# Performance work log

Hardware: AMD Instinct MI355X
Metric: run time of the kernel (lower is better)

Reference implementation:

```python
import jax, jax.numpy as jnp
import numpy as np

N_NODES = 100000
N_EDGES = 500000
NODE_IN = 16
HID = 128
EDGE_IN = 1
NUM_STACKED = 4  # layers 1..4 share shapes; layer 0 maps NODE_IN -> HID


def setup_inputs() -> dict:
    key = jax.random.key(0)
    ks = jax.random.split(key, 16)

    def p(k, shape, fan_in):
        return (jax.random.normal(k, shape, dtype=jnp.float32) / np.float32(np.sqrt(fan_in)))

    inp = {}
    inp["x"] = jax.random.normal(ks[0], (N_NODES, NODE_IN), dtype=jnp.float32)
    inp["edge_index"] = jax.random.randint(ks[1], (2, N_EDGES), 0, N_NODES)
    inp["edge_attr"] = jax.random.normal(ks[2], (N_EDGES, EDGE_IN), dtype=jnp.float32)
    # GINE layer 0 (NODE_IN -> HID): edge lin maps EDGE_IN -> NODE_IN (PyG GINEConv.lin)
    inp["We0"] = p(ks[3], (EDGE_IN, NODE_IN), EDGE_IN)
    inp["be0"] = jnp.zeros((NODE_IN,), jnp.float32)
    inp["W10"] = p(ks[4], (NODE_IN, HID), NODE_IN)
    inp["b10"] = jnp.zeros((HID,), jnp.float32)
    inp["W20"] = p(ks[5], (HID, HID), HID)
    inp["b20"] = jnp.zeros((HID,), jnp.float32)
    # GINE layers 1..4 (HID -> HID), stacked on leading axis
    inp["We_s"] = p(ks[6], (NUM_STACKED, EDGE_IN, HID), EDGE_IN)
    inp["be_s"] = jnp.zeros((NUM_STACKED, HID), jnp.float32)
    inp["W1_s"] = p(ks[7], (NUM_STACKED, HID, HID), HID)
    inp["b1_s"] = jnp.zeros((NUM_STACKED, HID), jnp.float32)
    inp["W2_s"] = p(ks[8], (NUM_STACKED, HID, HID), HID)
    inp["b2_s"] = jnp.zeros((NUM_STACKED, HID), jnp.float32)
    # edge predictor: Linear(2*HID, HID) -> ELU -> Linear(HID, 1)
    inp["Wp1"] = p(ks[9], (2 * HID, HID), 2 * HID)
    inp["bp1"] = jnp.zeros((HID,), jnp.float32)
    inp["Wp2"] = p(ks[10], (HID, 1), HID)
    inp["bp2"] = jnp.zeros((1,), jnp.float32)
    return inp


def _gine(x, src, dst, eattr, We, be, W1, b1, W2, b2):
    # PyG GINEConv: aggr_i = sum_{(j->i)} ReLU(x_j + lin(edge_attr)); out = nn((1+eps)*x + aggr), eps=0
    m = jax.nn.relu(x[src] + eattr @ We + be)                 # [E, d] gathered messages
    aggr = jax.ops.segment_sum(m, dst, num_segments=x.shape[0])  # scatter-add to targets
    h = x + aggr
    return jax.nn.elu(h @ W1 + b1) @ W2 + b2                  # nn = Linear-ELU-Linear


def reference(x, edge_index, edge_attr, We0, be0, W10, b10, W20, b20,
              We_s, be_s, W1_s, b1_s, W2_s, b2_s, Wp1, bp1, Wp2, bp2):
    src, dst = edge_index[0], edge_index[1]
    # dropout is identity at inference (eval mode)
    h = jax.nn.elu(_gine(x, src, dst, edge_attr, We0, be0, W10, b10, W20, b20))
    for l in range(NUM_STACKED):
        h = jax.nn.elu(_gine(h, src, dst, edge_attr,
                             We_s[l], be_s[l], W1_s[l], b1_s[l], W2_s[l], b2_s[l]))
    ef = jnp.concatenate([h[src], h[dst]], axis=1)            # [E, 2*HID]
    out = jax.nn.elu(ef @ Wp1 + bp1) @ Wp2 + bp2              # [E, 1]
    return out[:, 0]
```

## Files before the change

kernel.cpp:

```cpp
#include <hip/hip_runtime.h>

#define N_NODES 100000
#define N_EDGES 500000
#define NODE_IN 16
#define HID 128
#define LPAD 140
#define SCAN_CHUNK 1024
#define NB_SCAN ((N_NODES + SCAN_CHUNK - 1) / SCAN_CHUNK)

typedef __attribute__((ext_vector_type(8))) short short8;
typedef __attribute__((ext_vector_type(4))) float f32x4;

__device__ __forceinline__ float elu_f(float v) {
    return v > 0.f ? v : __expf(v) - 1.f;
}

__device__ __forceinline__ unsigned short f2b(float f) {
    unsigned int u = __float_as_uint(f);
    unsigned int r = (u + 0x7fffu + ((u >> 16) & 1u)) >> 16;
    return (unsigned short)r;
}
__device__ __forceinline__ float b2f(unsigned short h) {
    return __uint_as_float((unsigned int)h << 16);
}
__device__ __forceinline__ unsigned short f2h(float f) {
    _Float16 h = (_Float16)f;
    unsigned short u;
    __builtin_memcpy(&u, &h, 2);
    return u;
}
__device__ __forceinline__ float h2f(unsigned short u) {
    _Float16 h;
    __builtin_memcpy(&h, &u, 2);
    return (float)h;
}

__global__ void deg_count_kernel(const int* __restrict__ ei, int* __restrict__ deg) {
    int e = blockIdx.x * 256 + threadIdx.x;
    if (e < N_EDGES) atomicAdd(&deg[ei[N_EDGES + e]], 1);
}

__global__ __launch_bounds__(1024) void scanA_kernel(const int* __restrict__ deg, int* __restrict__ bsum) {
    __shared__ int s[SCAN_CHUNK];
    int i = blockIdx.x * SCAN_CHUNK + threadIdx.x;
    s[threadIdx.x] = (i < N_NODES) ? deg[i] : 0;
    __syncthreads();
    for (int off = SCAN_CHUNK / 2; off > 0; off >>= 1) {
        if (threadIdx.x < off) s[threadIdx.x] += s[threadIdx.x + off];
        __syncthreads();
    }
    if (threadIdx.x == 0) bsum[blockIdx.x] = s[0];
}

__global__ void scanB_kernel(const int* __restrict__ bsum, int* __restrict__ boff,
                             int* __restrict__ rowPtr) {
    if (threadIdx.x == 0 && blockIdx.x == 0) {
        int r = 0;
        for (int i = 0; i < NB_SCAN; i++) { boff[i] = r; r += bsum[i]; }
        rowPtr[N_NODES] = N_EDGES;
    }
}

__global__ __launch_bounds__(1024) void scanC_kernel(const int* __restrict__ deg,
                                                     const int* __restrict__ boff,
                                                     int* __restrict__ rowPtr,
                                                     int* __restrict__ cursor) {
    __shared__ int bufA[SCAN_CHUNK], bufB[SCAN_CHUNK];
    int i = blockIdx.x * SCAN_CHUNK + threadIdx.x;
    int t = threadIdx.x;
    bufA[t] = (i < N_NODES) ? deg[i] : 0;
    __syncthreads();
    int* src = bufA; int* dst = bufB;
    for (int off = 1; off < SCAN_CHUNK; off <<= 1) {
        dst[t] = (t >= off) ? (src[t - off] + src[t]) : src[t];
        __syncthreads();
        int* tmp = src; src = dst; dst = tmp;
    }
    if (i < N_NODES) {
        int excl = (t == 0) ? 0 : src[t - 1];
        int v = excl + boff[blockIdx.x];
        rowPtr[i] = v;
        cursor[i] = v;
    }
}

__global__ void fill_kernel(const int* __restrict__ ei, const float* __restrict__ ea,
                            int* __restrict__ cursor, int2* __restrict__ edgeP) {
    int e = blockIdx.x * 256 + threadIdx.x;
    if (e < N_EDGES) {
        int d = ei[N_EDGES + e];
        int p = atomicAdd(&cursor[d], 1);
        edgeP[p] = make_int2(ei[e], __float_as_int(ea[e]));
    }
}

__global__ __launch_bounds__(256) void pack_w_kernel(const float* __restrict__ W, int K_off,
                                                     unsigned short* __restrict__ hi,
                                                     unsigned short* __restrict__ lo)
{
    int gid = blockIdx.x * 256 + threadIdx.x;
    if (gid >= 4 * 8 * 64) return;
    int lane = gid & 63, tl = (gid >> 6) & 7, ch = gid >> 9;
    int kb = ch * 32 + (lane >> 4) * 8;
    int n  = tl * 16 + (lane & 15);
    for (int j = 0; j < 8; j++) {
        float w = W[(size_t)(K_off + kb + j) * 128 + n];
        unsigned short h = f2b(w);
        hi[(size_t)gid * 8 + j] = h;
        lo[(size_t)gid * 8 + j] = f2b(w - b2f(h));
    }
}

__global__ __launch_bounds__(256) void scatter0_kernel(
    const float* __restrict__ x, const int* __restrict__ ei,
    const float* __restrict__ ea, const float* __restrict__ We0,
    const float* __restrict__ be0, float* __restrict__ aggr)
{
    int idx = blockIdx.x * 256 + threadIdx.x;
    int e = idx >> 4, c = idx & 15;
    int s = ei[e], d = ei[N_EDGES + e];
    float m = x[s * NODE_IN + c] + ea[e] * We0[c] + be0[c];
    m = fmaxf(m, 0.f);
    atomicAdd(&aggr[d * NODE_IN + c], m);
}

__device__ __forceinline__ void fma4x4(float (&acc)[4][4],
    const float4& r0, const float4& r1, const float4& r2, const float4& r3,
    const float4& w0, const float4& w1, const float4& w2, const float4& w3)
{
    float r[4][4] = {{r0.x, r0.y, r0.z, r0.w}, {r1.x, r1.y, r1.z, r1.w},
                     {r2.x, r2.y, r2.z, r2.w}, {r3.x, r3.y, r3.z, r3.w}};
    float w[4][4] = {{w0.x, w0.y, w0.z, w0.w}, {w1.x, w1.y, w1.z, w1.w},
                     {w2.x, w2.y, w2.z, w2.w}, {w3.x, w3.y, w3.z, w3.w}};
#pragma unroll
    for (int i = 0; i < 4; i++)
#pragma unroll
        for (int k = 0; k < 4; k++)
#pragma unroll
            for (int c = 0; c < 4; c++)
                acc[i][c] = fmaf(r[i][k], w[k][c], acc[i][c]);
}

__global__ __launch_bounds__(256) void mlp0_kernel(
    const float* __restrict__ x, const float* __restrict__ aggr,
    const float* __restrict__ W1, const float* __restrict__ b1,
    const float* __restrict__ W2, const float* __restrict__ b2,
    unsigned short* __restrict__ h)
{
    __shared__ float in0[32][20];
    __shared__ float mid[32][HID];
    const int t = threadIdx.x;
    const int q = t & 31, g = t >> 5;
    const int c0 = q * 4;
    const int base = blockIdx.x * 32;

    for (int i = t; i < 32 * NODE_IN; i += 256) {
        int r = i >> 4, cc = i & 15;
        int n = base + r;
        in0[r][cc] = x[n * NODE_IN + cc] + aggr[n * NODE_IN + cc];
    }
    __syncthreads();

    float4 bb = *(const float4*)&b1[c0];
    float acc[4][4];
#pragma unroll
    for (int i = 0; i < 4; i++) { acc[i][0] = bb.x; acc[i][1] = bb.y; acc[i][2] = bb.z; acc[i][3] = bb.w; }
    for (int k = 0; k < NODE_IN; k += 4) {
        float4 r0 = *(const float4*)&in0[g * 4 + 0][k];
        float4 r1 = *(const float4*)&in0[g * 4 + 1][k];
        float4 r2 = *(const float4*)&in0[g * 4 + 2][k];
        float4 r3 = *(const float4*)&in0[g * 4 + 3][k];
        float4 w0 = *(const float4*)&W1[(k + 0) * HID + c0];
        float4 w1 = *(const float4*)&W1[(k + 1) * HID + c0];
        float4 w2 = *(const float4*)&W1[(k + 2) * HID + c0];
        float4 w3 = *(const float4*)&W1[(k + 3) * HID + c0];
        fma4x4(acc, r0, r1, r2, r3, w0, w1, w2, w3);
    }
#pragma unroll
    for (int i = 0; i < 4; i++)
        *(float4*)&mid[g * 4 + i][c0] = make_float4(elu_f(acc[i][0]), elu_f(acc[i][1]),
                                                    elu_f(acc[i][2]), elu_f(acc[i][3]));
    __syncthreads();

    float4 bb2 = *(const float4*)&b2[c0];
    float acc2[4][4];
#pragma unroll
    for (int i = 0; i < 4; i++) { acc2[i][0] = bb2.x; acc2[i][1] = bb2.y; acc2[i][2] = bb2.z; acc2[i][3] = bb2.w; }
    for (int k = 0; k < HID; k += 4) {
        float4 r0 = *(const float4*)&mid[g * 4 + 0][k];
        float4 r1 = *(const float4*)&mid[g * 4 + 1][k];
        float4 r2 = *(const float4*)&mid[g * 4 + 2][k];
        float4 r3 = *(const float4*)&mid[g * 4 + 3][k];
        float4 w0 = *(const float4*)&W2[(k + 0) * HID + c0];
        float4 w1 = *(const float4*)&W2[(k + 1) * HID + c0];
        float4 w2 = *(const float4*)&W2[(k + 2) * HID + c0];
        float4 w3 = *(const float4*)&W2[(k + 3) * HID + c0];
        fma4x4(acc2, r0, r1, r2, r3, w0, w1, w2, w3);
    }
#pragma unroll
    for (int i = 0; i < 4; i++) {
        ushort4 o;
        o.x = f2h(elu_f(acc2[i][0])); o.y = f2h(elu_f(acc2[i][1]));
        o.z = f2h(elu_f(acc2[i][2])); o.w = f2h(elu_f(acc2[i][3]));
        *(ushort4*)&h[(size_t)(base + g * 4 + i) * HID + c0] = o;
    }
}

__device__ __forceinline__ void afrag_split(const float (&buf)[16][LPAD], int lane,
                                            short8 (&ah)[4], short8 (&al)[4])
{
    const int m = lane & 15, s8 = (lane >> 4) * 8;
#pragma unroll
    for (int ch = 0; ch < 4; ch++) {
        float4 a0 = *(const float4*)&buf[m][ch * 32 + s8];
        float4 a1 = *(const float4*)&buf[m][ch * 32 + s8 + 4];
        float av[8] = {a0.x, a0.y, a0.z, a0.w, a1.x, a1.y, a1.z, a1.w};
#pragma unroll
        for (int j = 0; j < 8; j++) {
            unsigned short h = f2b(av[j]);
            ah[ch][j] = (short)h;
            al[ch][j] = (short)f2b(av[j] - b2f(h));
        }
    }
}

template <bool PRED>
__global__ __launch_bounds__(64) void gine_mfma_kernel(
    const unsigned short* __restrict__ hin, const int* __restrict__ rowPtr,
    const int2* __restrict__ edgeP,
    const float* __restrict__ We, const float* __restrict__ be,
    const unsigned short* __restrict__ W1h, const unsigned short* __restrict__ W1l,
    const float* __restrict__ b1,
    const unsigned short* __restrict__ W2h, const unsigned short* __restrict__ W2l,
    const float* __restrict__ b2,
    unsigned short* __restrict__ hout,
    const unsigned short* __restrict__ P1h, const unsigned short* __restrict__ P1l,
    const unsigned short* __restrict__ P2h, const unsigned short* __restrict__ P2l,
    unsigned short* __restrict__ Pbuf)
{
    __shared__ float buf[16][LPAD];
    const int lane = threadIdx.x;
    const int qg = lane & 15, rg = lane >> 4;
    const int c0 = qg * 8;
    const int base = blockIdx.x * 16;

    float wev[8], bev[8];
#pragma unroll
    for (int j = 0; j < 8; j++) { wev[j] = We[c0 + j]; bev[j] = be[c0 + j]; }

    int s0[4], e0[4];
    float acc[4][8];
#pragma unroll
    for (int i = 0; i < 4; i++) {
        int n = base + rg * 4 + i;
        s0[i] = rowPtr[n];
        e0[i] = rowPtr[n + 1];
        short8 h0 = *(const short8*)&hin[(size_t)n * HID + c0];
#pragma unroll
        for (int j = 0; j < 8; j++) acc[i][j] = h2f((unsigned short)h0[j]);
    }
    int maxd = 0;
#pragma unroll
    for (int i = 0; i < 4; i++) maxd = max(maxd, e0[i] - s0[i]);

    int idx[8]; float av[8]; bool act[8];
#pragma unroll
    for (int u = 0; u < 2; u++)
#pragma unroll
        for (int i = 0; i < 4; i++) {
            int slot = u * 4 + i;
            int j = s0[i] + u;
            act[slot] = j < e0[i];
            int jc = act[slot] ? j : (N_EDGES - 1);
            int2 ep = edgeP[jc];
            idx[slot] = ep.x;
            av[slot]  = __int_as_float(ep.y);
        }

    for (int sb = 0; sb < maxd; sb += 2) {
        short8 hraw[8];
#pragma unroll
        for (int s = 0; s < 8; s++)
            hraw[s] = *(const short8*)&hin[(size_t)idx[s] * HID + c0];

        int nidx[8]; float nav[8]; bool nact[8];
#pragma unroll
        for (int u = 0; u < 2; u++)
#pragma unroll
            for (int i = 0; i < 4; i++) {
                int slot = u * 4 + i;
                int j = s0[i] + sb + 2 + u;
                nact[slot] = j < e0[i];
                int jc = nact[slot] ? j : (N_EDGES - 1);
                int2 ep = edgeP[jc];
                nidx[slot] = ep.x;
                nav[slot]  = __int_as_float(ep.y);
            }

#pragma unroll
        for (int u = 0; u < 2; u++)
#pragma unroll
            for (int i = 0; i < 4; i++) {
                int slot = u * 4 + i;
                if (act[slot]) {
#pragma unroll
                    for (int j = 0; j < 8; j++) {
                        float hv = h2f((unsigned short)hraw[slot][j]);
                        acc[i][j] += fmaxf(fmaf(av[slot], wev[j], bev[j]) + hv, 0.f);
                    }
                }
            }
#pragma unroll
        for (int s = 0; s < 8; s++) {
            idx[s] = nidx[s]; av[s] = nav[s]; act[s] = nact[s];
        }
    }
#pragma unroll
    for (int i = 0; i < 4; i++) {
        *(float4*)&buf[rg * 4 + i][c0]     = make_float4(acc[i][0], acc[i][1], acc[i][2], acc[i][3]);
        *(float4*)&buf[rg * 4 + i][c0 + 4] = make_float4(acc[i][4], acc[i][5], acc[i][6], acc[i][7]);
    }
    __syncthreads();

    const int col16 = lane & 15, r0 = (lane >> 4) * 4;

    {
        short8 ah[4], al[4];
        afrag_split(buf, lane, ah, al);
        float res[8][4];
#pragma unroll
        for (int tl = 0; tl < 8; tl++) {
            int col = tl * 16 + col16;
            float bv = b1[col];
            f32x4 c = {bv, bv, bv, bv};
#pragma unroll
            for (int ch = 0; ch < 4; ch++) {
                int off = ((ch * 8 + tl) * 64 + lane) * 8;
                short8 bh = *(const short8*)&W1h[off];
                short8 bl = *(const short8*)&W1l[off];
                c = __builtin_amdgcn_mfma_f32_16x16x32_bf16(ah[ch], bh, c, 0, 0, 0);
                c = __builtin_amdgcn_mfma_f32_16x16x32_bf16(al[ch], bh, c, 0, 0, 0);
                c = __builtin_amdgcn_mfma_f32_16x16x32_bf16(ah[ch], bl, c, 0, 0, 0);
            }
#pragma unroll
            for (int r = 0; r < 4; r++) res[tl][r] = elu_f(c[r]);
        }
        __syncthreads();
#pragma unroll
        for (int tl = 0; tl < 8; tl++)
#pragma unroll
            for (int r = 0; r < 4; r++)
                buf[r0 + r][tl * 16 + col16] = res[tl][r];
    }
    __syncthreads();

    {
        short8 ah[4], al[4];
        afrag_split(buf, lane, ah, al);
        float res[8][4];
#pragma unroll
        for (int tl = 0; tl < 8; tl++) {
            int col = tl * 16 + col16;
            float bv = b2[col];
            f32x4 c = {bv, bv, bv, bv};
#pragma unroll
            for (int ch = 0; ch < 4; ch++) {
                int off = ((ch * 8 + tl) * 64 + lane) * 8;
                short8 bh = *(const short8*)&W2h[off];
                short8 bl = *(const short8*)&W2l[off];
                c = __builtin_amdgcn_mfma_f32_16x16x32_bf16(ah[ch], bh, c, 0, 0, 0);
                c = __builtin_amdgcn_mfma_f32_16x16x32_bf16(al[ch], bh, c, 0, 0, 0);
                c = __builtin_amdgcn_mfma_f32_16x16x32_bf16(ah[ch], bl, c, 0, 0, 0);
            }
#pragma unroll
            for (int r = 0; r < 4; r++) res[tl][r] = elu_f(c[r]);
        }
        __syncthreads();
#pragma unroll
        for (int tl = 0; tl < 8; tl++)
#pragma unroll
            for (int r = 0; r < 4; r++)
                buf[r0 + r][tl * 16 + col16] = res[tl][r];
    }
    __syncthreads();

    if constexpr (!PRED) {
#pragma unroll
        for (int i = 0; i < 4; i++) {
            int n = base + rg * 4 + i;
            short8 o;
#pragma unroll
            for (int j = 0; j < 8; j++) o[j] = (short)f2h(buf[rg * 4 + i][c0 + j]);
            *(short8*)&hout[(size_t)n * HID + c0] = o;
        }
    } else {
        short8 ah[4], al[4];
        afrag_split(buf, lane, ah, al);
#pragma unroll
        for (int tl = 0; tl < 8; tl++) {
            int col = tl * 16 + col16;
            f32x4 c1 = {0.f, 0.f, 0.f, 0.f};
            f32x4 c2 = {0.f, 0.f, 0.f, 0.f};
#pragma unroll
            for (int ch = 0; ch < 4; ch++) {
                int off = ((ch * 8 + tl) * 64 + lane) * 8;
                short8 bh1 = *(const short8*)&P1h[off];
                short8 bl1 = *(const short8*)&P1l[off];
                c1 = __builtin_amdgcn_mfma_f32_16x16x32_bf16(ah[ch], bh1, c1, 0, 0, 0);
                c1 = __builtin_amdgcn_mfma_f32_16x16x32_bf16(al[ch], bh1, c1, 0, 0, 0);
                c1 = __builtin_amdgcn_mfma_f32_16x16x32_bf16(ah[ch], bl1, c1, 0, 0, 0);
                short8 bh2 = *(const short8*)&P2h[off];
                short8 bl2 = *(const short8*)&P2l[off];
                c2 = __builtin_amdgcn_mfma_f32_16x16x32_bf16(ah[ch], bh2, c2, 0, 0, 0);
                c2 = __builtin_amdgcn_mfma_f32_16x16x32_bf16(al[ch], bh2, c2, 0, 0, 0);
                c2 = __builtin_amdgcn_mfma_f32_16x16x32_bf16(ah[ch], bl2, c2, 0, 0, 0);
            }
#pragma unroll
            for (int r = 0; r < 4; r++) {
                size_t n = base + r0 + r;
                Pbuf[n * 256 + col]       = f2b(c1[r]);
                Pbuf[n * 256 + 128 + col] = f2b(c2[r]);
            }
        }
    }
}

__global__ __launch_bounds__(256) void pred_edge_kernel(
    const unsigned short* __restrict__ Pbuf, const int* __restrict__ ei,
    const float* __restrict__ bp1, const float* __restrict__ Wp2,
    const float* __restrict__ bp2, float* __restrict__ out)
{
    const int t = threadIdx.x;
    const int lane = t & 31;
    const int eloc = t >> 5;
    const int e = blockIdx.x * 8 + eloc;
    const int c0 = lane * 4;

    int s = ei[e], d = ei[N_EDGES + e];
    ushort4 ua = *(const ushort4*)&Pbuf[(size_t)s * 256 + c0];
    ushort4 ub = *(const ushort4*)&Pbuf[(size_t)d * 256 + 128 + c0];
    float4 bb = *(const float4*)&bp1[c0];
    float4 w = *(const float4*)&Wp2[c0];
    float r = elu_f(b2f(ua.x) + b2f(ub.x) + bb.x) * w.x
            + elu_f(b2f(ua.y) + b2f(ub.y) + bb.y) * w.y
            + elu_f(b2f(ua.z) + b2f(ub.z) + bb.z) * w.z
            + elu_f(b2f(ua.w) + b2f(ub.w) + bb.w) * w.w;
#pragma unroll
    for (int off = 16; off > 0; off >>= 1) r += __shfl_down(r, off, 32);
    if (lane == 0) out[e] = r + bp2[0];
}

extern "C" void kernel_launch(void* const* d_in, const int* in_sizes, int n_in,
                              void* d_out, int out_size, void* d_ws, size_t ws_size,
                              hipStream_t stream) {
    const float* x    = (const float*)d_in[0];
    const int*   ei   = (const int*)d_in[1];
    const float* ea   = (const float*)d_in[2];
    const float* We0  = (const float*)d_in[3];
    const float* be0  = (const float*)d_in[4];
    const float* W10  = (const float*)d_in[5];
    const float* b10  = (const float*)d_in[6];
    const float* W20  = (const float*)d_in[7];
    const float* b20  = (const float*)d_in[8];
    const float* We_s = (const float*)d_in[9];
    const float* be_s = (const float*)d_in[10];
    const float* W1_s = (const float*)d_in[11];
    const float* b1_s = (const float*)d_in[12];
    const float* W2_s = (const float*)d_in[13];
    const float* b2_s = (const float*)d_in[14];
    const float* Wp1  = (const float*)d_in[15];
    const float* bp1  = (const float*)d_in[16];
    const float* Wp2  = (const float*)d_in[17];
    const float* bp2  = (const float*)d_in[18];
    float* out = (float*)d_out;

    unsigned short* h16A = (unsigned short*)d_ws;
    unsigned short* h16B = h16A + (size_t)N_NODES * HID;
    unsigned short* Pbuf = h16B + (size_t)N_NODES * HID;
    float* R = (float*)(Pbuf + (size_t)N_NODES * 256);

    float* aggr0 = R;
    int* deg     = (int*)(aggr0 + (size_t)N_NODES * NODE_IN);
    int* rowPtr  = deg + N_NODES;
    int* cursor  = rowPtr + N_NODES + 1;
    int2* edgeP  = (int2*)(cursor + N_NODES);
    int* bsum    = (int*)(edgeP + N_EDGES);
    int* boff    = bsum + NB_SCAN;

    unsigned short* wpk = (unsigned short*)(R + (size_t)6 * 1024 * 1024);
    const size_t WSLOT = 16384;

    hipMemsetAsync(deg, 0, N_NODES * sizeof(int), stream);
    deg_count_kernel<<<(N_EDGES + 255) / 256, 256, 0, stream>>>(ei, deg);
    scanA_kernel<<<NB_SCAN, SCAN_CHUNK, 0, stream>>>(deg, bsum);
    scanB_kernel<<<1, 64, 0, stream>>>(bsum, boff, rowPtr);
    scanC_kernel<<<NB_SCAN, SCAN_CHUNK, 0, stream>>>(deg, boff, rowPtr, cursor);
    fill_kernel<<<(N_EDGES + 255) / 256, 256, 0, stream>>>(ei, ea, cursor, edgeP);

    for (int l = 0; l < 4; l++) {
        pack_w_kernel<<<8, 256, 0, stream>>>(W1_s + (size_t)l * 16384, 0,
                                             wpk + (0 + l) * WSLOT, wpk + (4 + l) * WSLOT);
        pack_w_kernel<<<8, 256, 0, stream>>>(W2_s + (size_t)l * 16384, 0,
                                             wpk + (8 + l) * WSLOT, wpk + (12 + l) * WSLOT);
    }
    pack_w_kernel<<<8, 256, 0, stream>>>(Wp1, 0,   wpk + 16 * WSLOT, wpk + 17 * WSLOT);
    pack_w_kernel<<<8, 256, 0, stream>>>(Wp1, 128, wpk + 18 * WSLOT, wpk + 19 * WSLOT);

    hipMemsetAsync(aggr0, 0, (size_t)N_NODES * NODE_IN * sizeof(float), stream);
    scatter0_kernel<<<(N_EDGES * NODE_IN) / 256, 256, 0, stream>>>(x, ei, ea, We0, be0, aggr0);
    mlp0_kernel<<<N_NODES / 32, 256, 0, stream>>>(x, aggr0, W10, b10, W20, b20, h16A);

    unsigned short* hin = h16A; unsigned short* hout_ = h16B;
    for (int l = 0; l < 3; l++) {
        gine_mfma_kernel<false><<<N_NODES / 16, 64, 0, stream>>>(
            hin, rowPtr, edgeP,
            We_s + l * HID, be_s + l * HID,
            wpk + (0 + l) * WSLOT, wpk + (4 + l) * WSLOT, b1_s + l * HID,
            wpk + (8 + l) * WSLOT, wpk + (12 + l) * WSLOT, b2_s + l * HID,
            hout_, nullptr, nullptr, nullptr, nullptr, nullptr);
        unsigned short* tmp = hin; hin = hout_; hout_ = tmp;
    }

    {
        const int l = 3;
        gine_mfma_kernel<true><<<N_NODES / 16, 64, 0, stream>>>(
            hin, rowPtr, edgeP,
            We_s + l * HID, be_s + l * HID,
            wpk + (0 + l) * WSLOT, wpk + (4 + l) * WSLOT, b1_s + l * HID,
            wpk + (8 + l) * WSLOT, wpk + (12 + l) * WSLOT, b2_s + l * HID,
            nullptr, wpk + 16 * WSLOT, wpk + 17 * WSLOT,
            wpk + 18 * WSLOT, wpk + 19 * WSLOT, Pbuf);
    }

    pred_edge_kernel<<<N_EDGES / 8, 256, 0, stream>>>(Pbuf, ei, bp1, Wp2, bp2, out);
}
```

Before: 616.8 us.

## Sort nodes by in-degree so each GINE block gathers balanced edge counts

Builds a degree histogram, scans it, and produces a permutation that groups nodes by in-degree. The GINE kernels then process nodes in permuted order, so the four nodes sharing a wavefront row group have similar degrees and the maxd loop wastes fewer iterations. This adds three small preprocessing kernels plus a memset, and it makes hin/hout and Pbuf row accesses indirect and scattered rather than contiguous, which costs memory locality.

```diff
diff --git a/kernel.cpp b/kernel.cpp
--- a/kernel.cpp
+++ b/kernel.cpp
@@ -7,6 +7,7 @@
 #define LPAD 140
 #define SCAN_CHUNK 1024
 #define NB_SCAN ((N_NODES + SCAN_CHUNK - 1) / SCAN_CHUNK)
+#define DBINS 1024
 
 typedef __attribute__((ext_vector_type(8))) short short8;
 typedef __attribute__((ext_vector_type(4))) float f32x4;
@@ -91,6 +92,36 @@
         int d = ei[N_EDGES + e];
         int p = atomicAdd(&cursor[d], 1);
         edgeP[p] = make_int2(ei[e], __float_as_int(ea[e]));
+    }
+}
+
+__global__ void hist_kernel(const int* __restrict__ deg, int* __restrict__ hist) {
+    int i = blockIdx.x * 256 + threadIdx.x;
+    if (i < N_NODES) atomicAdd(&hist[min(deg[i], DBINS - 1)], 1);
+}
+
+__global__ __launch_bounds__(1024) void binscan_kernel(const int* __restrict__ hist,
+                                                       int* __restrict__ bcur) {
+    __shared__ int bufA[DBINS], bufB[DBINS];
+    int t = threadIdx.x;
+    bufA[t] = hist[t];
+    __syncthreads();
+    int* src = bufA; int* dst = bufB;
+    for (int off = 1; off < DBINS; off <<= 1) {
+        dst[t] = (t >= off) ? (src[t - off] + src[t]) : src[t];
+        __syncthreads();
+        int* tmp = src; src = dst; dst = tmp;
+    }
+    bcur[t] = (t == 0) ? 0 : src[t - 1];
+}
+
+__global__ void permute_kernel(const int* __restrict__ deg, int* __restrict__ bcur,
+                               int* __restrict__ perm) {
+    int i = blockIdx.x * 256 + threadIdx.x;
+    if (i < N_NODES) {
+        int b = min(deg[i], DBINS - 1);
+        int p = atomicAdd(&bcur[b], 1);
+        perm[p] = i;
     }
 }
 
@@ -227,7 +258,7 @@
 template <bool PRED>
 __global__ __launch_bounds__(64) void gine_mfma_kernel(
     const unsigned short* __restrict__ hin, const int* __restrict__ rowPtr,
-    const int2* __restrict__ edgeP,
+    const int2* __restrict__ edgeP, const int* __restrict__ perm,
     const float* __restrict__ We, const float* __restrict__ be,
     const unsigned short* __restrict__ W1h, const unsigned short* __restrict__ W1l,
     const float* __restrict__ b1,
@@ -248,14 +279,14 @@
 #pragma unroll
     for (int j = 0; j < 8; j++) { wev[j] = We[c0 + j]; bev[j] = be[c0 + j]; }
 
-    int s0[4], e0[4];
+    int nn[4], s0[4], e0[4];
     float acc[4][8];
 #pragma unroll
     for (int i = 0; i < 4; i++) {
-        int n = base + rg * 4 + i;
-        s0[i] = rowPtr[n];
-        e0[i] = rowPtr[n + 1];
-        short8 h0 = *(const short8*)&hin[(size_t)n * HID + c0];
+        nn[i] = perm[base + rg * 4 + i];
+        s0[i] = rowPtr[nn[i]];
+        e0[i] = rowPtr[nn[i] + 1];
+        short8 h0 = *(const short8*)&hin[(size_t)nn[i] * HID + c0];
 #pragma unroll
         for (int j = 0; j < 8; j++) acc[i][j] = h2f((unsigned short)h0[j]);
     }
@@ -387,15 +418,17 @@
     if constexpr (!PRED) {
 #pragma unroll
         for (int i = 0; i < 4; i++) {
-            int n = base + rg * 4 + i;
             short8 o;
 #pragma unroll
             for (int j = 0; j < 8; j++) o[j] = (short)f2h(buf[rg * 4 + i][c0 + j]);
-            *(short8*)&hout[(size_t)n * HID + c0] = o;
+            *(short8*)&hout[(size_t)nn[i] * HID + c0] = o;
         }
     } else {
         short8 ah[4], al[4];
         afrag_split(buf, lane, ah, al);
+        int pn[4];
+#pragma unroll
+        for (int r = 0; r < 4; r++) pn[r] = perm[base + r0 + r];
 #pragma unroll
         for (int tl = 0; tl < 8; tl++) {
             int col = tl * 16 + col16;
@@ -417,7 +450,7 @@
             }
 #pragma unroll
             for (int r = 0; r < 4; r++) {
-                size_t n = base + r0 + r;
+                size_t n = (size_t)pn[r];
                 Pbuf[n * 256 + col]       = f2b(c1[r]);
                 Pbuf[n * 256 + 128 + col] = f2b(c2[r]);
             }
@@ -486,6 +519,9 @@
     int2* edgeP  = (int2*)(cursor + N_NODES);
     int* bsum    = (int*)(edgeP + N_EDGES);
     int* boff    = bsum + NB_SCAN;
+    int* hist    = boff + NB_SCAN;
+    int* bcur    = hist + DBINS;
+    int* perm    = bcur + DBINS;
 
     unsigned short* wpk = (unsigned short*)(R + (size_t)6 * 1024 * 1024);
     const size_t WSLOT = 16384;
@@ -497,6 +533,11 @@
     scanC_kernel<<<NB_SCAN, SCAN_CHUNK, 0, stream>>>(deg, boff, rowPtr, cursor);
     fill_kernel<<<(N_EDGES + 255) / 256, 256, 0, stream>>>(ei, ea, cursor, edgeP);
 
+    hipMemsetAsync(hist, 0, DBINS * sizeof(int), stream);
+    hist_kernel<<<(N_NODES + 255) / 256, 256, 0, stream>>>(deg, hist);
+    binscan_kernel<<<1, DBINS, 0, stream>>>(hist, bcur);
+    permute_kernel<<<(N_NODES + 255) / 256, 256, 0, stream>>>(deg, bcur, perm);
+
     for (int l = 0; l < 4; l++) {
         pack_w_kernel<<<8, 256, 0, stream>>>(W1_s + (size_t)l * 16384, 0,
                                              wpk + (0 + l) * WSLOT, wpk + (4 + l) * WSLOT);
@@ -513,7 +554,7 @@
     unsigned short* hin = h16A; unsigned short* hout_ = h16B;
     for (int l = 0; l < 3; l++) {
         gine_mfma_kernel<false><<<N_NODES / 16, 64, 0, stream>>>(
-            hin, rowPtr, edgeP,
+            hin, rowPtr, edgeP, perm,
             We_s + l * HID, be_s + l * HID,
             wpk + (0 + l) * WSLOT, wpk + (4 + l) * WSLOT, b1_s + l * HID,
             wpk + (8 + l) * WSLOT, wpk + (12 + l) * WSLOT, b2_s + l * HID,
@@ -524,7 +565,7 @@
     {
         const int l = 3;
         gine_mfma_kernel<true><<<N_NODES / 16, 64, 0, stream>>>(
-            hin, rowPtr, edgeP,
+            hin, rowPtr, edgeP, perm,
             We_s + l * HID, be_s + l * HID,
             wpk + (0 + l) * WSLOT, wpk + (4 + l) * WSLOT, b1_s + l * HID,
             wpk + (8 + l) * WSLOT, wpk + (12 + l) * WSLOT, b2_s + l * HID,
```

New measurement: 1.392 ms. 2.26x slower.
